# Performance work log

Hardware: AMD Instinct MI355X
Metric: run time of the kernel (lower is better)

The kernel has to match this reference:

```python
import jax, jax.numpy as jnp
import numpy as np

# dims: B batch, T max obs steps, D sensors (input_size), H hidden_dim, P prep_hidden
B, T, D, H, P = 512, 64, 32, 512, 32
COV, COVH, PH = 64, 128, 128
MIXING = 0.1
LOG2PI = float(np.log(2.0 * np.pi))  # == 2 * log(sqrt(2*pi))
OBS_STD = 0.01


def setup_inputs() -> dict:
    key = jax.random.key(0)
    ks = jax.random.split(key, 20)
    times = jnp.sort(jax.random.uniform(ks[0], (B, T), dtype=jnp.float32), axis=1)
    # ragged counts in [T//2, T]; force max == T so the loop length matches torch's max(num_obs)
    num_obs = jax.random.randint(ks[1], (B,), T // 2, T + 1).at[0].set(T)
    X = jax.random.normal(ks[2], (B, T, D), dtype=jnp.float32)
    M = (jax.random.uniform(ks[3], (B, T, D)) < 0.8).astype(jnp.float32)
    cov = jax.random.normal(ks[4], (B, COV), dtype=jnp.float32)
    delta_t = jnp.full((1,), 0.05, jnp.float32)

    def lin(i, fi, fo):
        w = (jax.random.normal(ks[i], (fi, fo)) / np.sqrt(fi)).astype(jnp.float32)
        b = jnp.full((fo,), 0.05, jnp.float32)
        return w, b

    cov_w1, cov_b1 = lin(5, COV, COVH)
    cov_w2, cov_b2 = lin(6, COVH, H)
    p_w1, p_b1 = lin(7, H, PH)
    p_w2, p_b2 = lin(8, PH, 2 * D)
    ode_whr = (jax.random.normal(ks[9], (H, H)) / np.sqrt(H)).astype(jnp.float32)
    ode_whz = (jax.random.normal(ks[10], (H, H)) / np.sqrt(H)).astype(jnp.float32)
    ode_whh = (jax.random.normal(ks[11], (H, H)) / np.sqrt(H)).astype(jnp.float32)
    wprep = (np.sqrt(2.0 / (4 + P)) * jax.random.normal(ks[12], (D, 4, P))).astype(jnp.float32)
    bprep = jnp.full((D, P), 0.1, jnp.float32)
    gru_wih = (jax.random.normal(ks[13], (3 * H, P * D)) / np.sqrt(P * D)).astype(jnp.float32)
    gru_whh = (jax.random.normal(ks[14], (3 * H, H)) / np.sqrt(H)).astype(jnp.float32)
    gru_bih = jnp.zeros((3 * H,), jnp.float32)
    gru_bhh = jnp.zeros((3 * H,), jnp.float32)
    return dict(times=times, X=X, M=M, cov=cov, delta_t=delta_t,
                cov_w1=cov_w1, cov_b1=cov_b1, cov_w2=cov_w2, cov_b2=cov_b2,
                p_w1=p_w1, p_b1=p_b1, p_w2=p_w2, p_b2=p_b2,
                ode_whr=ode_whr, ode_whz=ode_whz, ode_whh=ode_whh,
                wprep=wprep, bprep=bprep,
                gru_wih=gru_wih, gru_whh=gru_whh, gru_bih=gru_bih, gru_bhh=gru_bhh,
                num_obs=num_obs)


def reference(times, X, M, cov, delta_t,
              cov_w1, cov_b1, cov_w2, cov_b2,
              p_w1, p_b1, p_w2, p_b2,
              ode_whr, ode_whz, ode_whh,
              wprep, bprep,
              gru_wih, gru_whh, gru_bih, gru_bhh,
              num_obs):
    def p_model(h):
        return jax.nn.relu(h @ p_w1 + p_b1) @ p_w2 + p_b2

    # covariates_map: Linear-ReLU-Linear-Tanh
    h0 = jnp.tanh(jax.nn.relu(cov @ cov_w1 + cov_b1) @ cov_w2 + cov_b2)  # [B, H]
    mask_all = (num_obs[None, :] > jnp.arange(T)[:, None]).astype(jnp.float32)  # [T, B]
    xs = (times.T, jnp.transpose(X, (1, 0, 2)), jnp.transpose(M, (1, 0, 2)), mask_all)

    def step(carry, xs_t):
        h, last_t, l1, l2 = carry
        t_cur, Xc, Mc, m = xs_t  # [B], [B,D], [B,D], [B]
        diff = (t_cur - last_t) * m  # zero for inactive rows -> ODE no-op
        # FullGRUODECell_Autonomous, single explicit Euler step with dt = diff
        r = jax.nn.sigmoid(h @ ode_whr.T)
        z = jax.nn.sigmoid(h @ ode_whz.T)
        u = jnp.tanh((r * h) @ ode_whh.T)
        h = h + (1.0 - z) * (u - h) * diff[:, None]
        # observation NLL (GRUObservationCellLogvar)
        p = p_model(h)
        mean, logvar = p[:, :D], p[:, D:]
        sigma = jnp.exp(0.5 * logvar)
        error = (Xc - mean) / sigma
        losses = 0.5 * (error ** 2 + logvar + LOG2PI) * Mc * m[:, None]  # [B, D]
        nll = jnp.sum(losses) / jnp.maximum(jnp.sum(m) * D, 1.0)
        # prep features: stack([X, mean, logvar, error]) @ w_prep + bias, relu, mask
        feats = jnp.stack([Xc, mean, logvar, error], axis=2)  # [B, D, 4]
        xp = jax.nn.relu(jnp.einsum('bdf,dfp->bdp', feats, wprep) + bprep) * Mc[:, :, None]
        xp = xp.reshape(-1, D * P)  # [B, D*P]
        # torch GRUCell (gate order r, z, n), applied only to observed rows
        gi = xp @ gru_wih.T + gru_bih
        gh = h @ gru_whh.T + gru_bhh
        rg = jax.nn.sigmoid(gi[:, :H] + gh[:, :H])
        zg = jax.nn.sigmoid(gi[:, H:2 * H] + gh[:, H:2 * H])
        ng = jnp.tanh(gi[:, 2 * H:] + rg * gh[:, 2 * H:])
        h_new = (1.0 - zg) * ng + zg * h
        h = jnp.where(m[:, None] > 0, h_new, h)
        # KL loss against obs noise (compute_KL_loss, logvar=True)
        p2 = p_model(h)
        mean2, logvar2 = p2[:, :D], p2[:, D:]
        std2 = jnp.exp(0.5 * logvar2)
        kl = (jnp.log(jnp.float32(OBS_STD)) - 0.5 * logvar2
              + (std2 ** 2 + (mean2 - Xc) ** 2) / (2.0 * OBS_STD ** 2) - 0.5)
        l1 = l1 + jnp.sum(losses)
        l2 = l2 + jnp.sum(kl * Mc * m[:, None])
        last_t = jnp.where(m > 0, t_cur, last_t)
        return (h, last_t, l1, l2), nll

    init = (h0, jnp.zeros((B,), jnp.float32), jnp.float32(0.0), jnp.float32(0.0))
    (h, _, l1, l2), nlls = jax.lax.scan(step, init, xs)
    loss = l1 + MIXING * l2
    return h, loss, jnp.mean(nlls), l1, l2
```

## Files before the change

kernel.cpp:

```cpp
#include <hip/hip_runtime.h>

typedef unsigned short u16;
typedef unsigned int u32;
typedef unsigned long long u64;
typedef __attribute__((ext_vector_type(8))) short short8;
typedef __attribute__((ext_vector_type(4))) float floatx4;

#define MFMA16(a,b,c) __builtin_amdgcn_mfma_f32_16x16x32_bf16((a),(b),(c),0,0,0)

#define B_ 512
#define T_ 64
#define D_ 32
#define H_ 512

#define OFF_WHR  0
#define OFF_WHZ  262144
#define OFF_WHH  524288
#define OFF_GWHH 786432
#define OFF_GWIH 1572864
#define OFF_PW1T 3145728
#define OFF_PW2T 3211264
#define WS_ELEMS 3219456
#define GBUF     3219456
#define GSTRIDE  32768
#define HG_OFF   0
#define RHG_OFF  8192
#define XPG_OFF  16384
#define CTR_BYTE 8536064
#define CLAIM_BYTE (CTR_BYTE + 2048)

#define LOG2PI_f 1.8378770664093453f
#define LOGOBS_f -4.605170185988091f
#define INV2OBS_f 5000.0f
#define SCAL_OFF 262144

#define AT_ST32(p,v) __hip_atomic_store((p),(v),__ATOMIC_RELAXED,__HIP_MEMORY_SCOPE_AGENT)
#define AT_ST64(p,v) __hip_atomic_store((p),(v),__ATOMIC_RELAXED,__HIP_MEMORY_SCOPE_AGENT)
#define AT_LD64(p)   __hip_atomic_load((p),__ATOMIC_RELAXED,__HIP_MEMORY_SCOPE_AGENT)

__device__ __forceinline__ u16 f2bf(float f) {
  union { float f; unsigned u; } v; v.f = f;
  unsigned r = v.u + 0x7FFFu + ((v.u >> 16) & 1u);
  return (u16)(r >> 16);
}
__device__ __forceinline__ u32 pack2(float a, float b) {
  return (u32)f2bf(a) | ((u32)f2bf(b) << 16);
}
__device__ __forceinline__ float sigm(float x) { return 1.f / (1.f + expf(-x)); }

__device__ __forceinline__ short8 ldA(const u16* buf, int rowB, int row, int kE) {
  int byte = row * rowB + (((kE << 1)) ^ ((row & 7) << 4));
  return *(const short8*)((const char*)buf + byte);
}

__global__ void convw(const float* __restrict__ whr, const float* __restrict__ whz,
                      const float* __restrict__ whh, const float* __restrict__ gwhh,
                      const float* __restrict__ gwih, const float* __restrict__ pw1,
                      const float* __restrict__ pw2, u16* __restrict__ ws) {
  int i = blockIdx.x * 256 + threadIdx.x;
  if (i >= WS_ELEMS) return;
  float v;
  if (i < OFF_WHZ) v = whr[i];
  else if (i < OFF_GWHH) {
    if (i < OFF_WHH) v = whz[i - OFF_WHZ];
    else v = whh[i - OFF_WHH];
  } else if (i < OFF_GWIH) v = gwhh[i - OFF_GWHH];
  else if (i < OFF_PW1T) v = gwih[i - OFF_GWIH];
  else if (i < OFF_PW2T) { int l = i - OFF_PW1T; int j = l >> 9, k = l & 511; v = pw1[k * 128 + j]; }
  else { int l = i - OFF_PW2T; int j = l >> 7, k = l & 127; v = pw2[k * 64 + j]; }
  ws[i] = f2bf(v);
}

__device__ __forceinline__ void group_barrier(u32* ctr, unsigned* ep) {
  asm volatile("s_waitcnt vmcnt(0)" ::: "memory");
  __syncthreads();
  unsigned target = 8u * (++(*ep));
  if (threadIdx.x == 0) {
    __hip_atomic_fetch_add(ctr, 1u, __ATOMIC_RELAXED, __HIP_MEMORY_SCOPE_AGENT);
    while (__hip_atomic_load(ctr, __ATOMIC_RELAXED, __HIP_MEMORY_SCOPE_AGENT) < target)
      __builtin_amdgcn_s_sleep(1);
  }
  __syncthreads();
}

__global__ __launch_bounds__(512, 2)
void nnfo_main(const float* __restrict__ times, const float* __restrict__ Xg,
               const float* __restrict__ Mgl, const float* __restrict__ cov,
               const float* __restrict__ cov_w1, const float* __restrict__ cov_b1,
               const float* __restrict__ cov_w2, const float* __restrict__ cov_b2,
               const float* __restrict__ p_b1, const float* __restrict__ p_b2,
               const float* __restrict__ wprep, const float* __restrict__ bprep,
               const float* __restrict__ gru_bih, const float* __restrict__ gru_bhh,
               const int* __restrict__ num_obs, u16* __restrict__ ws,
               float* __restrict__ out) {
  __shared__ u16 bufA[8192];
  __shared__ u16 xpL[16384];
  __shared__ float accbuf[8192];
  __shared__ u16 hid1A[2048];
  __shared__ float pbuf[1024];
  __shared__ float h_own[1024];
  __shared__ float zbuf[1024];
  __shared__ float invden[T_];
  __shared__ float mr16[16], df16[16], lt16[16];
  __shared__ int nobs16[16];
  __shared__ float redbuf[24];
  __shared__ int gs_sh[2];

  const int tid = threadIdx.x;
  const int wv = tid >> 6;
  const int lane = tid & 63;
  const int colc = lane & 15;
  const int khalf = lane >> 4;
  const int rowc = khalf << 2;

  if (tid == 0) {
    unsigned xcc;
    asm volatile("s_getreg_b32 %0, hwreg(HW_REG_XCC_ID)" : "=s"(xcc));
    xcc &= 7u;
    u32* claim = (u32*)((char*)ws + CLAIM_BYTE);
    unsigned c = __hip_atomic_fetch_add(&claim[xcc], 1u, __ATOMIC_RELAXED,
                                        __HIP_MEMORY_SCOPE_AGENT);
    gs_sh[0] = (int)(c & 31u);
    gs_sh[1] = (int)xcc;
  }
  __syncthreads();
  const int g = gs_sh[0];
  const int s = gs_sh[1];
  const int b0 = g << 4;

  const u16* Whr  = ws + OFF_WHR;
  const u16* Whz  = ws + OFF_WHZ;
  const u16* Whh  = ws + OFF_WHH;
  const u16* Gwhh = ws + OFF_GWHH;
  const u16* Gwih = ws + OFF_GWIH;
  const u16* Pw1T = ws + OFF_PW1T;
  const u16* Pw2T = ws + OFF_PW2T;
  u16* hg  = ws + GBUF + g * GSTRIDE + HG_OFF;
  u16* rhg = ws + GBUF + g * GSTRIDE + RHG_OFF;
  u16* xpg = ws + GBUF + g * GSTRIDE + XPG_OFF;
  u32* ctr = (u32*)((char*)ws + CTR_BYTE) + g * 16;
  unsigned ep = 0;

  for (int t = tid; t < T_; t += 512) {
    int cnt = 0;
    for (int b = 0; b < B_; ++b) cnt += (num_obs[b] > t) ? 1 : 0;
    invden[t] = 1.0f / fmaxf((float)cnt * (float)D_, 1.0f);
  }
  if (tid < 16) { nobs16[tid] = num_obs[b0 + tid]; lt16[tid] = 0.f; }
  for (int i = tid; i < 16 * 64; i += 512) {
    int m = i >> 6, k = i & 63;
    pbuf[i] = cov[(b0 + m) * 64 + k];
  }
  __syncthreads();
  for (int i = tid; i < 16 * 128; i += 512) {
    int m = i >> 7, j = i & 127;
    float sacc = cov_b1[j];
    for (int k = 0; k < 64; ++k) sacc += pbuf[m * 64 + k] * cov_w1[k * 128 + j];
    accbuf[i] = fmaxf(sacc, 0.f);
  }
  __syncthreads();
  {
    int row = tid >> 5, colb = (tid & 31) << 4;
    for (int c = 0; c < 16; ++c) {
      int col = colb + c;
      float sacc = cov_b2[col];
      for (int k = 0; k < 128; ++k) sacc += accbuf[row * 128 + k] * cov_w2[k * 512 + col];
      float v = tanhf(sacc);
      int byte = (row << 10) | (((col << 1)) ^ ((row & 7) << 4));
      *(u16*)((char*)bufA + byte) = f2bf(v);
      if ((col >> 6) == s) h_own[row * 64 + (col & 63)] = v;
    }
  }
  float l1a = 0.f, l2a = 0.f, nlla = 0.f;
  float Xc_s = 0.f, Mc_s = 0.f;
  __syncthreads();

  const int row_l = tid >> 5;
  const int dloc  = (tid >> 3) & 3;
  const int pq    = tid & 7;
  const int d_l   = (s << 2) + dloc;
  const int cp    = tid & 31;

  for (int t = 0; t < T_; ++t) {
    if (tid < 16) {
      float tcv = times[(b0 + tid) * T_ + t];
      float mm = (t < nobs16[tid]) ? 1.f : 0.f;
      df16[tid] = (tcv - lt16[tid]) * mm;
      mr16[tid] = mm;
      lt16[tid] = (mm > 0.f) ? tcv : lt16[tid];
    }
    {
      int mat = wv >> 2, jt = wv & 3;
      int colg = (s << 6) + (jt << 4) + colc;
      const u16* W = (mat ? Whz : Whr) + colg * 512;
      floatx4 acc = (floatx4){0.f,0.f,0.f,0.f};
      #pragma unroll
      for (int kc = 0; kc < 16; ++kc) {
        int kE = (kc << 5) + (khalf << 3);
        acc = MFMA16(ldA(bufA, 1024, colc, kE), *(const short8*)(W + kE), acc);
      }
      #pragma unroll
      for (int i = 0; i < 4; ++i)
        accbuf[mat * 1024 + (rowc + i) * 64 + (jt << 4) + colc] = acc[i];
    }
    __syncthreads();
    {
      int p0 = (row_l << 6) + (cp << 1);
      float rv0 = sigm(accbuf[p0]);
      float rv1 = sigm(accbuf[p0 + 1]);
      zbuf[p0]     = sigm(accbuf[1024 + p0]);
      zbuf[p0 + 1] = sigm(accbuf[1024 + p0 + 1]);
      AT_ST32((u32*)(rhg + (row_l << 9) + (s << 6) + (cp << 1)),
              pack2(rv0 * h_own[p0], rv1 * h_own[p0 + 1]));
    }
    group_barrier(ctr, &ep);
    {
      u64 tmp[4];
      #pragma unroll
      for (int i = 0; i < 4; ++i) tmp[i] = AT_LD64((const u64*)rhg + tid + 512 * i);
      #pragma unroll
      for (int i = 0; i < 4; ++i) {
        int e = (tid + 512 * i) << 2;
        int row = e >> 9, col = e & 511;
        *(u64*)((char*)bufA + (row << 10) + (((col << 1)) ^ ((row & 7) << 4))) = tmp[i];
      }
    }
    __syncthreads();
    {
      int jt = wv & 3, kh = wv >> 2;
      int colg = (s << 6) + (jt << 4) + colc;
      const u16* W = Whh + colg * 512;
      floatx4 acc = (floatx4){0.f,0.f,0.f,0.f};
      #pragma unroll
      for (int kc = kh * 8; kc < kh * 8 + 8; ++kc) {
        int kE = (kc << 5) + (khalf << 3);
        acc = MFMA16(ldA(bufA, 1024, colc, kE), *(const short8*)(W + kE), acc);
      }
      #pragma unroll
      for (int i = 0; i < 4; ++i)
        accbuf[kh * 1024 + (rowc + i) * 64 + (jt << 4) + colc] = acc[i];
    }
    __syncthreads();
    {
      int p0 = (row_l << 6) + (cp << 1);
      float u0 = tanhf(accbuf[p0] + accbuf[1024 + p0]);
      float u1 = tanhf(accbuf[p0 + 1] + accbuf[1024 + p0 + 1]);
      float h0v = h_own[p0], h1v = h_own[p0 + 1];
      float dd = df16[row_l];
      float hn0 = h0v + (1.f - zbuf[p0]) * (u0 - h0v) * dd;
      float hn1 = h1v + (1.f - zbuf[p0 + 1]) * (u1 - h1v) * dd;
      h_own[p0] = hn0; h_own[p0 + 1] = hn1;
      AT_ST32((u32*)(hg + (row_l << 9) + (s << 6) + (cp << 1)), pack2(hn0, hn1));
    }
    group_barrier(ctr, &ep);
    {
      u64 tmp[4];
      #pragma unroll
      for (int i = 0; i < 4; ++i) tmp[i] = AT_LD64((const u64*)hg + tid + 512 * i);
      #pragma unroll
      for (int i = 0; i < 4; ++i) {
        int e = (tid + 512 * i) << 2;
        int row = e >> 9, col = e & 511;
        *(u64*)((char*)bufA + (row << 10) + (((col << 1)) ^ ((row & 7) << 4))) = tmp[i];
      }
    }
    __syncthreads();
    {
      int colg = (wv << 4) + colc;
      const u16* W = Pw1T + colg * 512;
      floatx4 acc = (floatx4){0.f,0.f,0.f,0.f};
      #pragma unroll
      for (int kc = 0; kc < 16; ++kc) {
        int kE = (kc << 5) + (khalf << 3);
        acc = MFMA16(ldA(bufA, 1024, colc, kE), *(const short8*)(W + kE), acc);
      }
      float bias = p_b1[colg];
      #pragma unroll
      for (int i = 0; i < 4; ++i) {
        int row = rowc + i;
        float v = fmaxf(acc[i] + bias, 0.f);
        *(u16*)((char*)hid1A + ((row << 8) | (((colg << 1)) ^ ((row & 7) << 4)))) = f2bf(v);
      }
    }
    __syncthreads();
    if (wv < 4) {
      int colg = (wv << 4) + colc;
      const u16* W = Pw2T + colg * 128;
      floatx4 acc = (floatx4){0.f,0.f,0.f,0.f};
      #pragma unroll
      for (int kc = 0; kc < 4; ++kc) {
        int kE = (kc << 5) + (khalf << 3);
        acc = MFMA16(ldA(hid1A, 256, colc, kE), *(const short8*)(W + kE), acc);
      }
      float bias = p_b2[colg];
      #pragma unroll
      for (int i = 0; i < 4; ++i) pbuf[(rowc + i) * 64 + colg] = acc[i] + bias;
    }
    __syncthreads();
    {
      float mean = pbuf[row_l * 64 + d_l];
      float logvar = pbuf[row_l * 64 + 32 + d_l];
      size_t xoff = ((size_t)(b0 + row_l) * T_ + t) * D_ + d_l;
      Xc_s = Xg[xoff];
      Mc_s = Mgl[xoff];
      float mm = mr16[row_l];
      float sg = expf(0.5f * logvar);
      float err = (Xc_s - mean) / sg;
      if (pq == 0) {
        float lv = 0.5f * (err * err + logvar + LOG2PI_f) * Mc_s * mm;
        l1a += lv;
        nlla += lv * invden[t];
      }
      const float* wp = wprep + d_l * 128;
      const float* bp = bprep + d_l * 32;
      float xv[4];
      #pragma unroll
      for (int k = 0; k < 4; ++k) {
        int pi = (pq << 2) + k;
        float v = bp[pi] + Xc_s * wp[pi] + mean * wp[32 + pi] + logvar * wp[64 + pi] + err * wp[96 + pi];
        xv[k] = fmaxf(v, 0.f) * Mc_s;
      }
      u64 packed = (u64)pack2(xv[0], xv[1]) | ((u64)pack2(xv[2], xv[3]) << 32);
      AT_ST64((u64*)(xpg + (row_l << 10) + (s << 7) + (dloc << 5) + (pq << 2)), packed);
    }
    group_barrier(ctr, &ep);
    {
      u64 tmp[8];
      #pragma unroll
      for (int i = 0; i < 8; ++i) tmp[i] = AT_LD64((const u64*)xpg + tid + 512 * i);
      #pragma unroll
      for (int i = 0; i < 8; ++i) {
        int e = (tid + 512 * i) << 2;
        int row = e >> 10, col = e & 1023;
        *(u64*)((char*)xpL + (row << 11) + (((col << 1)) ^ ((row & 7) << 4))) = tmp[i];
      }
    }
    __syncthreads();
    {
      int jt = wv & 3, kh = wv >> 2;
      int colg = (s << 6) + (jt << 4) + colc;
      const u16* bw = Gwhh + colg * 512;
      const u16* bi = Gwih + colg * 1024;
      floatx4 ar = (floatx4){0.f,0.f,0.f,0.f}, az = ar, an = ar, ah = ar;
      #pragma unroll
      for (int kc = kh * 8; kc < kh * 8 + 8; ++kc) {
        int kE = (kc << 5) + (khalf << 3);
        short8 a = ldA(bufA, 1024, colc, kE);
        ar = MFMA16(a, *(const short8*)(bw + kE), ar);
        az = MFMA16(a, *(const short8*)(bw + 262144 + kE), az);
        ah = MFMA16(a, *(const short8*)(bw + 524288 + kE), ah);
      }
      #pragma unroll
      for (int kc = kh * 16; kc < kh * 16 + 16; ++kc) {
        int kE = (kc << 5) + (khalf << 3);
        short8 a = ldA(xpL, 2048, colc, kE);
        ar = MFMA16(a, *(const short8*)(bi + kE), ar);
        az = MFMA16(a, *(const short8*)(bi + 524288 + kE), az);
        an = MFMA16(a, *(const short8*)(bi + 1048576 + kE), an);
      }
      #pragma unroll
      for (int i = 0; i < 4; ++i) {
        int idx = (rowc + i) * 64 + (jt << 4) + colc;
        accbuf[(0 + kh) * 1024 + idx] = ar[i];
        accbuf[(2 + kh) * 1024 + idx] = az[i];
        accbuf[(4 + kh) * 1024 + idx] = an[i];
        accbuf[(6 + kh) * 1024 + idx] = ah[i];
      }
    }
    __syncthreads();
    {
      int p0 = (row_l << 6) + (cp << 1);
      float hn[2];
      float mm = mr16[row_l];
      #pragma unroll
      for (int q = 0; q < 2; ++q) {
        int p = p0 + q;
        int j = (s << 6) + (cp << 1) + q;
        float Arr = accbuf[p] + accbuf[1024 + p];
        float Azz = accbuf[2048 + p] + accbuf[3072 + p];
        float Ann = accbuf[4096 + p] + accbuf[5120 + p];
        float Ahh = accbuf[6144 + p] + accbuf[7168 + p];
        float rg = sigm(Arr + gru_bih[j] + gru_bhh[j]);
        float zg = sigm(Azz + gru_bih[512 + j] + gru_bhh[512 + j]);
        float ng = tanhf(Ann + gru_bih[1024 + j] + rg * (Ahh + gru_bhh[1024 + j]));
        float h = h_own[p];
        float hv = (1.f - zg) * ng + zg * h;
        hv = (mm > 0.f) ? hv : h;
        h_own[p] = hv;
        hn[q] = hv;
      }
      AT_ST32((u32*)(hg + (row_l << 9) + (s << 6) + (cp << 1)), pack2(hn[0], hn[1]));
    }
    group_barrier(ctr, &ep);
    {
      u64 tmp[4];
      #pragma unroll
      for (int i = 0; i < 4; ++i) tmp[i] = AT_LD64((const u64*)hg + tid + 512 * i);
      #pragma unroll
      for (int i = 0; i < 4; ++i) {
        int e = (tid + 512 * i) << 2;
        int row = e >> 9, col = e & 511;
        *(u64*)((char*)bufA + (row << 10) + (((col << 1)) ^ ((row & 7) << 4))) = tmp[i];
      }
    }
    __syncthreads();
    {
      int colg = (wv << 4) + colc;
      const u16* W = Pw1T + colg * 512;
      floatx4 acc = (floatx4){0.f,0.f,0.f,0.f};
      #pragma unroll
      for (int kc = 0; kc < 16; ++kc) {
        int kE = (kc << 5) + (khalf << 3);
        acc = MFMA16(ldA(bufA, 1024, colc, kE), *(const short8*)(W + kE), acc);
      }
      float bias = p_b1[colg];
      #pragma unroll
      for (int i = 0; i < 4; ++i) {
        int row = rowc + i;
        float v = fmaxf(acc[i] + bias, 0.f);
        *(u16*)((char*)hid1A + ((row << 8) | (((colg << 1)) ^ ((row & 7) << 4)))) = f2bf(v);
      }
    }
    __syncthreads();
    if (wv < 4) {
      int colg = (wv << 4) + colc;
      const u16* W = Pw2T + colg * 128;
      floatx4 acc = (floatx4){0.f,0.f,0.f,0.f};
      #pragma unroll
      for (int kc = 0; kc < 4; ++kc) {
        int kE = (kc << 5) + (khalf << 3);
        acc = MFMA16(ldA(hid1A, 256, colc, kE), *(const short8*)(W + kE), acc);
      }
      float bias = p_b2[colg];
      #pragma unroll
      for (int i = 0; i < 4; ++i) pbuf[(rowc + i) * 64 + colg] = acc[i] + bias;
    }
    __syncthreads();
    if (pq == 0) {
      float mean2 = pbuf[row_l * 64 + d_l];
      float logvar2 = pbuf[row_l * 64 + 32 + d_l];
      float s2 = expf(logvar2);
      float dm = mean2 - Xc_s;
      float kl = LOGOBS_f - 0.5f * logvar2 + (s2 + dm * dm) * INV2OBS_f - 0.5f;
      l2a += kl * Mc_s * mr16[row_l];
    }
    __syncthreads();
  }

  for (int pos = tid; pos < 1024; pos += 512) {
    int row = pos >> 6, cl = pos & 63;
    out[(size_t)(b0 + row) * H_ + (s << 6) + cl] = h_own[pos];
  }
  #pragma unroll
  for (int off = 32; off > 0; off >>= 1) {
    l1a += __shfl_down(l1a, off, 64);
    l2a += __shfl_down(l2a, off, 64);
    nlla += __shfl_down(nlla, off, 64);
  }
  if (lane == 0) { redbuf[wv] = l1a; redbuf[8 + wv] = l2a; redbuf[16 + wv] = nlla; }
  __syncthreads();
  if (tid == 0) {
    float L1 = 0.f, L2 = 0.f, NL = 0.f;
    for (int w = 0; w < 8; ++w) { L1 += redbuf[w]; L2 += redbuf[8 + w]; NL += redbuf[16 + w]; }
    atomicAdd(out + SCAL_OFF + 0, L1 + 0.1f * L2);
    atomicAdd(out + SCAL_OFF + 1, NL * (1.f / 64.f));
    atomicAdd(out + SCAL_OFF + 2, L1);
    atomicAdd(out + SCAL_OFF + 3, L2);
  }
}

extern "C" void kernel_launch(void* const* d_in, const int* in_sizes, int n_in,
                              void* d_out, int out_size, void* d_ws, size_t ws_size,
                              hipStream_t stream) {
  const float* times  = (const float*)d_in[0];
  const float* X      = (const float*)d_in[1];
  const float* M      = (const float*)d_in[2];
  const float* cov    = (const float*)d_in[3];
  const float* cov_w1 = (const float*)d_in[5];
  const float* cov_b1 = (const float*)d_in[6];
  const float* cov_w2 = (const float*)d_in[7];
  const float* cov_b2 = (const float*)d_in[8];
  const float* p_w1   = (const float*)d_in[9];
  const float* p_b1   = (const float*)d_in[10];
  const float* p_w2   = (const float*)d_in[11];
  const float* p_b2   = (const float*)d_in[12];
  const float* ode_whr = (const float*)d_in[13];
  const float* ode_whz = (const float*)d_in[14];
  const float* ode_whh = (const float*)d_in[15];
  const float* wprep  = (const float*)d_in[16];
  const float* bprep  = (const float*)d_in[17];
  const float* gru_wih = (const float*)d_in[18];
  const float* gru_whh = (const float*)d_in[19];
  const float* gru_bih = (const float*)d_in[20];
  const float* gru_bhh = (const float*)d_in[21];
  const int* num_obs  = (const int*)d_in[22];
  float* out = (float*)d_out;
  u16* ws = (u16*)d_ws;

  hipMemsetAsync(out + SCAL_OFF, 0, 4 * sizeof(float), stream);
  hipMemsetAsync((char*)d_ws + CTR_BYTE, 0, 2048 + 64, stream);
  convw<<<dim3((WS_ELEMS + 255) / 256), dim3(256), 0, stream>>>(
      ode_whr, ode_whz, ode_whh, gru_whh, gru_wih, p_w1, p_w2, ws);

  void* args[] = { (void*)&times, (void*)&X, (void*)&M, (void*)&cov,
                   (void*)&cov_w1, (void*)&cov_b1, (void*)&cov_w2, (void*)&cov_b2,
                   (void*)&p_b1, (void*)&p_b2, (void*)&wprep, (void*)&bprep,
                   (void*)&gru_bih, (void*)&gru_bhh, (void*)&num_obs, (void*)&ws,
                   (void*)&out };
  hipError_t e = hipLaunchCooperativeKernel((const void*)nnfo_main, dim3(256), dim3(512),
                                            args, 0, stream);
  if (e != hipSuccess) {
    nnfo_main<<<dim3(256), dim3(512), 0, stream>>>(
        times, X, M, cov, cov_w1, cov_b1, cov_w2, cov_b2,
        p_b1, p_b2, wprep, bprep, gru_bih, gru_bhh, num_obs, ws, out);
  }
}
```

Measured before the change: 3.992 ms.

## Split group barrier and overlap GRU hidden MFMAs with xp exchange

The group barrier is split into separate arrive and wait phases, so the GRU hidden-state matmul (Gwhh) now runs between publishing the prepped inputs and waiting for the other blocks. Exchange traffic through global memory moves from relaxed atomic 32/64-bit loads and stores to inline-asm dwordx4/dword stores and loads with sc0 sc1 cache bits, which halves or quarters the number of load instructions. The aim is to hide barrier latency behind compute and cut the instruction count of the exchange. It relies on the sc0 sc1 bits giving coherent visibility across CUs in place of the atomics' ordering guarantees.

After: 3.689 ms. -7.6%, faster.

```diff
diff --git a/kernel.cpp b/kernel.cpp
--- a/kernel.cpp
+++ b/kernel.cpp
@@ -5,6 +5,7 @@
 typedef unsigned long long u64;
 typedef __attribute__((ext_vector_type(8))) short short8;
 typedef __attribute__((ext_vector_type(4))) float floatx4;
+typedef __attribute__((ext_vector_type(4))) unsigned int u32x4;
 
 #define MFMA16(a,b,c) __builtin_amdgcn_mfma_f32_16x16x32_bf16((a),(b),(c),0,0,0)
 
@@ -34,10 +35,6 @@
 #define INV2OBS_f 5000.0f
 #define SCAL_OFF 262144
 
-#define AT_ST32(p,v) __hip_atomic_store((p),(v),__ATOMIC_RELAXED,__HIP_MEMORY_SCOPE_AGENT)
-#define AT_ST64(p,v) __hip_atomic_store((p),(v),__ATOMIC_RELAXED,__HIP_MEMORY_SCOPE_AGENT)
-#define AT_LD64(p)   __hip_atomic_load((p),__ATOMIC_RELAXED,__HIP_MEMORY_SCOPE_AGENT)
-
 __device__ __forceinline__ u16 f2bf(float f) {
   union { float f; unsigned u; } v; v.f = f;
   unsigned r = v.u + 0x7FFFu + ((v.u >> 16) & 1u);
@@ -47,6 +44,21 @@
   return (u32)f2bf(a) | ((u32)f2bf(b) << 16);
 }
 __device__ __forceinline__ float sigm(float x) { return 1.f / (1.f + expf(-x)); }
+
+__device__ __forceinline__ u32x4 ldg_cc16(const void* p) {
+  u32x4 r;
+  asm volatile("global_load_dwordx4 %0, %1, off sc0 sc1"
+               : "=v"(r) : "v"(p) : "memory");
+  return r;
+}
+__device__ __forceinline__ void stg_cc4(void* p, u32 v) {
+  asm volatile("global_store_dword %0, %1, off sc0 sc1"
+               :: "v"(p), "v"(v) : "memory");
+}
+__device__ __forceinline__ void stg_cc8(void* p, u64 v) {
+  asm volatile("global_store_dwordx2 %0, %1, off sc0 sc1"
+               :: "v"(p), "v"(v) : "memory");
+}
 
 __device__ __forceinline__ short8 ldA(const u16* buf, int rowB, int row, int kE) {
   int byte = row * rowB + (((kE << 1)) ^ ((row & 7) << 4));
@@ -71,12 +83,15 @@
   ws[i] = f2bf(v);
 }
 
-__device__ __forceinline__ void group_barrier(u32* ctr, unsigned* ep) {
+__device__ __forceinline__ void gb_arrive(u32* ctr) {
   asm volatile("s_waitcnt vmcnt(0)" ::: "memory");
   __syncthreads();
+  if (threadIdx.x == 0)
+    __hip_atomic_fetch_add(ctr, 1u, __ATOMIC_RELAXED, __HIP_MEMORY_SCOPE_AGENT);
+}
+__device__ __forceinline__ void gb_wait(u32* ctr, unsigned* ep) {
   unsigned target = 8u * (++(*ep));
   if (threadIdx.x == 0) {
-    __hip_atomic_fetch_add(ctr, 1u, __ATOMIC_RELAXED, __HIP_MEMORY_SCOPE_AGENT);
     while (__hip_atomic_load(ctr, __ATOMIC_RELAXED, __HIP_MEMORY_SCOPE_AGENT) < target)
       __builtin_amdgcn_s_sleep(1);
   }
@@ -180,6 +195,7 @@
   const int pq    = tid & 7;
   const int d_l   = (s << 2) + dloc;
   const int cp    = tid & 31;
+  const int jtG = wv & 3, khG = wv >> 2;
 
   for (int t = 0; t < T_; ++t) {
     if (tid < 16) {
@@ -210,20 +226,19 @@
       float rv1 = sigm(accbuf[p0 + 1]);
       zbuf[p0]     = sigm(accbuf[1024 + p0]);
       zbuf[p0 + 1] = sigm(accbuf[1024 + p0 + 1]);
-      AT_ST32((u32*)(rhg + (row_l << 9) + (s << 6) + (cp << 1)),
+      stg_cc4(rhg + (row_l << 9) + (s << 6) + (cp << 1),
               pack2(rv0 * h_own[p0], rv1 * h_own[p0 + 1]));
     }
-    group_barrier(ctr, &ep);
-    {
-      u64 tmp[4];
-      #pragma unroll
-      for (int i = 0; i < 4; ++i) tmp[i] = AT_LD64((const u64*)rhg + tid + 512 * i);
-      #pragma unroll
-      for (int i = 0; i < 4; ++i) {
-        int e = (tid + 512 * i) << 2;
-        int row = e >> 9, col = e & 511;
-        *(u64*)((char*)bufA + (row << 10) + (((col << 1)) ^ ((row & 7) << 4))) = tmp[i];
-      }
+    gb_arrive(ctr); gb_wait(ctr, &ep);
+    {
+      u32x4 t0 = ldg_cc16(rhg + (tid << 3));
+      u32x4 t1 = ldg_cc16(rhg + (tid << 3) + 4096);
+      asm volatile("s_waitcnt vmcnt(0)" ::: "memory");
+      __builtin_amdgcn_sched_barrier(0);
+      int c = tid, row = c >> 6, col = (c << 3) & 511;
+      *(u32x4*)((char*)bufA + (row << 10) + (((col << 1)) ^ ((row & 7) << 4))) = t0;
+      c = tid + 512; row = c >> 6; col = (c << 3) & 511;
+      *(u32x4*)((char*)bufA + (row << 10) + (((col << 1)) ^ ((row & 7) << 4))) = t1;
     }
     __syncthreads();
     {
@@ -250,19 +265,18 @@
       float hn0 = h0v + (1.f - zbuf[p0]) * (u0 - h0v) * dd;
       float hn1 = h1v + (1.f - zbuf[p0 + 1]) * (u1 - h1v) * dd;
       h_own[p0] = hn0; h_own[p0 + 1] = hn1;
-      AT_ST32((u32*)(hg + (row_l << 9) + (s << 6) + (cp << 1)), pack2(hn0, hn1));
-    }
-    group_barrier(ctr, &ep);
-    {
-      u64 tmp[4];
-      #pragma unroll
-      for (int i = 0; i < 4; ++i) tmp[i] = AT_LD64((const u64*)hg + tid + 512 * i);
-      #pragma unroll
-      for (int i = 0; i < 4; ++i) {
-        int e = (tid + 512 * i) << 2;
-        int row = e >> 9, col = e & 511;
-        *(u64*)((char*)bufA + (row << 10) + (((col << 1)) ^ ((row & 7) << 4))) = tmp[i];
-      }
+      stg_cc4(hg + (row_l << 9) + (s << 6) + (cp << 1), pack2(hn0, hn1));
+    }
+    gb_arrive(ctr); gb_wait(ctr, &ep);
+    {
+      u32x4 t0 = ldg_cc16(hg + (tid << 3));
+      u32x4 t1 = ldg_cc16(hg + (tid << 3) + 4096);
+      asm volatile("s_waitcnt vmcnt(0)" ::: "memory");
+      __builtin_amdgcn_sched_barrier(0);
+      int c = tid, row = c >> 6, col = (c << 3) & 511;
+      *(u32x4*)((char*)bufA + (row << 10) + (((col << 1)) ^ ((row & 7) << 4))) = t0;
+      c = tid + 512; row = c >> 6; col = (c << 3) & 511;
+      *(u32x4*)((char*)bufA + (row << 10) + (((col << 1)) ^ ((row & 7) << 4))) = t1;
     }
     __syncthreads();
     {
@@ -321,37 +335,45 @@
         xv[k] = fmaxf(v, 0.f) * Mc_s;
       }
       u64 packed = (u64)pack2(xv[0], xv[1]) | ((u64)pack2(xv[2], xv[3]) << 32);
-      AT_ST64((u64*)(xpg + (row_l << 10) + (s << 7) + (dloc << 5) + (pq << 2)), packed);
-    }
-    group_barrier(ctr, &ep);
-    {
-      u64 tmp[8];
-      #pragma unroll
-      for (int i = 0; i < 8; ++i) tmp[i] = AT_LD64((const u64*)xpg + tid + 512 * i);
-      #pragma unroll
-      for (int i = 0; i < 8; ++i) {
-        int e = (tid + 512 * i) << 2;
-        int row = e >> 10, col = e & 1023;
-        *(u64*)((char*)xpL + (row << 11) + (((col << 1)) ^ ((row & 7) << 4))) = tmp[i];
-      }
-    }
-    __syncthreads();
-    {
-      int jt = wv & 3, kh = wv >> 2;
-      int colg = (s << 6) + (jt << 4) + colc;
+      stg_cc8(xpg + (row_l << 10) + (s << 7) + (dloc << 5) + (pq << 2), packed);
+    }
+    gb_arrive(ctr);
+    floatx4 ar = (floatx4){0.f,0.f,0.f,0.f}, az = ar, an = ar, ah = ar;
+    {
+      int colg = (s << 6) + (jtG << 4) + colc;
       const u16* bw = Gwhh + colg * 512;
-      const u16* bi = Gwih + colg * 1024;
-      floatx4 ar = (floatx4){0.f,0.f,0.f,0.f}, az = ar, an = ar, ah = ar;
-      #pragma unroll
-      for (int kc = kh * 8; kc < kh * 8 + 8; ++kc) {
+      #pragma unroll
+      for (int kc = khG * 8; kc < khG * 8 + 8; ++kc) {
         int kE = (kc << 5) + (khalf << 3);
         short8 a = ldA(bufA, 1024, colc, kE);
         ar = MFMA16(a, *(const short8*)(bw + kE), ar);
         az = MFMA16(a, *(const short8*)(bw + 262144 + kE), az);
         ah = MFMA16(a, *(const short8*)(bw + 524288 + kE), ah);
       }
-      #pragma unroll
-      for (int kc = kh * 16; kc < kh * 16 + 16; ++kc) {
+    }
+    gb_wait(ctr, &ep);
+    {
+      u32x4 x0 = ldg_cc16(xpg + (tid << 3));
+      u32x4 x1 = ldg_cc16(xpg + (tid << 3) + 4096);
+      u32x4 x2 = ldg_cc16(xpg + (tid << 3) + 8192);
+      u32x4 x3 = ldg_cc16(xpg + (tid << 3) + 12288);
+      asm volatile("s_waitcnt vmcnt(0)" ::: "memory");
+      __builtin_amdgcn_sched_barrier(0);
+      int c = tid, row = c >> 7, col = (c << 3) & 1023;
+      *(u32x4*)((char*)xpL + (row << 11) + (((col << 1)) ^ ((row & 7) << 4))) = x0;
+      c = tid + 512; row = c >> 7; col = (c << 3) & 1023;
+      *(u32x4*)((char*)xpL + (row << 11) + (((col << 1)) ^ ((row & 7) << 4))) = x1;
+      c = tid + 1024; row = c >> 7; col = (c << 3) & 1023;
+      *(u32x4*)((char*)xpL + (row << 11) + (((col << 1)) ^ ((row & 7) << 4))) = x2;
+      c = tid + 1536; row = c >> 7; col = (c << 3) & 1023;
+      *(u32x4*)((char*)xpL + (row << 11) + (((col << 1)) ^ ((row & 7) << 4))) = x3;
+    }
+    __syncthreads();
+    {
+      int colg = (s << 6) + (jtG << 4) + colc;
+      const u16* bi = Gwih + colg * 1024;
+      #pragma unroll
+      for (int kc = khG * 16; kc < khG * 16 + 16; ++kc) {
         int kE = (kc << 5) + (khalf << 3);
         short8 a = ldA(xpL, 2048, colc, kE);
         ar = MFMA16(a, *(const short8*)(bi + kE), ar);
@@ -360,11 +382,11 @@
       }
       #pragma unroll
       for (int i = 0; i < 4; ++i) {
-        int idx = (rowc + i) * 64 + (jt << 4) + colc;
-        accbuf[(0 + kh) * 1024 + idx] = ar[i];
-        accbuf[(2 + kh) * 1024 + idx] = az[i];
-        accbuf[(4 + kh) * 1024 + idx] = an[i];
-        accbuf[(6 + kh) * 1024 + idx] = ah[i];
+        int idx = (rowc + i) * 64 + (jtG << 4) + colc;
+        accbuf[(0 + khG) * 1024 + idx] = ar[i];
+        accbuf[(2 + khG) * 1024 + idx] = az[i];
+        accbuf[(4 + khG) * 1024 + idx] = an[i];
+        accbuf[(6 + khG) * 1024 + idx] = ah[i];
       }
     }
     __syncthreads();
@@ -389,19 +411,18 @@
         h_own[p] = hv;
         hn[q] = hv;
       }
-      AT_ST32((u32*)(hg + (row_l << 9) + (s << 6) + (cp << 1)), pack2(hn[0], hn[1]));
-    }
-    group_barrier(ctr, &ep);
-    {
-      u64 tmp[4];
-      #pragma unroll
-      for (int i = 0; i < 4; ++i) tmp[i] = AT_LD64((const u64*)hg + tid + 512 * i);
-      #pragma unroll
-      for (int i = 0; i < 4; ++i) {
-        int e = (tid + 512 * i) << 2;
-        int row = e >> 9, col = e & 511;
-        *(u64*)((char*)bufA + (row << 10) + (((col << 1)) ^ ((row & 7) << 4))) = tmp[i];
-      }
+      stg_cc4(hg + (row_l << 9) + (s << 6) + (cp << 1), pack2(hn[0], hn[1]));
+    }
+    gb_arrive(ctr); gb_wait(ctr, &ep);
+    {
+      u32x4 t0 = ldg_cc16(hg + (tid << 3));
+      u32x4 t1 = ldg_cc16(hg + (tid << 3) + 4096);
+      asm volatile("s_waitcnt vmcnt(0)" ::: "memory");
+      __builtin_amdgcn_sched_barrier(0);
+      int c = tid, row = c >> 6, col = (c << 3) & 511;
+      *(u32x4*)((char*)bufA + (row << 10) + (((col << 1)) ^ ((row & 7) << 4))) = t0;
+      c = tid + 512; row = c >> 6; col = (c << 3) & 511;
+      *(u32x4*)((char*)bufA + (row << 10) + (((col << 1)) ^ ((row & 7) << 4))) = t1;
     }
     __syncthreads();
     {
```
